# Kernel tuning notes

Hardware: AMD Instinct MI355X
Metric: run time of the kernel (lower is better)

Reference implementation:

```python
import jax, jax.numpy as jnp
import numpy as np

N_NODES = 100000
N_EDGES = 1600000
IN_FEAT = 64
OUT_FEAT = 64


def setup_inputs() -> dict:
    key = jax.random.key(0)
    k_h, k_src, k_dst, k_w, k_b = jax.random.split(key, 5)
    h = jax.random.normal(k_h, (N_NODES, IN_FEAT), dtype=jnp.float32)
    src = jax.random.randint(k_src, (N_EDGES,), 0, N_NODES, dtype=jnp.int64)
    dst = jax.random.randint(k_dst, (N_EDGES,), 0, N_NODES, dtype=jnp.int64)
    # nn.Linear(in_feat*2, out_feat): weight [out, 2*in], bias [out]
    W = jax.random.normal(k_w, (OUT_FEAT, 2 * IN_FEAT), dtype=jnp.float32) * 0.05
    b = jax.random.normal(k_b, (OUT_FEAT,), dtype=jnp.float32) * 0.05
    return {"h": h, "src": src, "dst": dst, "W": W, "b": b}


def reference(h, src, dst, W, b):
    # message = copy_u: gather source-node features along edges  [E, F]
    msgs = h[src]
    # mean reduce per destination node (DGL mean -> 0 for isolated nodes)
    summed = jax.ops.segment_sum(msgs, dst, num_segments=N_NODES)  # [N, F]
    deg = jax.ops.segment_sum(jnp.ones((src.shape[0],), dtype=h.dtype), dst,
                              num_segments=N_NODES)                # [N]
    h_N = summed / jnp.maximum(deg, 1.0)[:, None]
    h_total = jnp.concatenate([h, h_N], axis=1)                    # [N, 2F]
    return h_total @ W.T + b
```

## Files before the change

### kernel.cpp

```cpp
#include <hip/hip_runtime.h>

#define IN_FEAT 64
#define OUT_FEAT 64
#define CAP 48
#define NB 196
#define BUFCAP 64
#define QPAD 16
#define ROUTE_BLOCKS 256

typedef __attribute__((ext_vector_type(8))) _Float16 half8;
typedef __attribute__((ext_vector_type(4))) float floatx4;
typedef __attribute__((ext_vector_type(4))) int intx4;

__global__ __launch_bounds__(256) void conv_kernel(const float* __restrict__ h,
        _Float16* __restrict__ h16, int total8, int* __restrict__ qtail) {
    int t = blockIdx.x * 256 + threadIdx.x;
    if (t < (NB * QPAD) / 4) ((intx4*)qtail)[t] = (intx4){0, 0, 0, 0};
    if (t >= total8) return;
    const float4* p = (const float4*)(h + (long long)t * 8);
    float4 a = p[0], c = p[1];
    half8 v;
    v[0] = (_Float16)a.x; v[1] = (_Float16)a.y;
    v[2] = (_Float16)a.z; v[3] = (_Float16)a.w;
    v[4] = (_Float16)c.x; v[5] = (_Float16)c.y;
    v[6] = (_Float16)c.z; v[7] = (_Float16)c.w;
    *(half8*)(h16 + (long long)t * 8) = v;
}

__global__ __launch_bounds__(512) void route_kernel(const int* __restrict__ src,
        const int* __restrict__ dst, int* __restrict__ qtail,
        int* __restrict__ queue, int E, int qcap, int epb) {
    __shared__ int cnt[NB];
    __shared__ int sbase[NB];
    __shared__ __align__(16) int buf[NB * BUFCAP];
    int tid = threadIdx.x;
    int eb = blockIdx.x * epb;
    int ee = eb + epb; if (ee > E) ee = E;
    for (int r0 = eb; r0 < ee; r0 += 512 * 8) {
        for (int i = tid; i < NB; i += 512) cnt[i] = 0;
        __syncthreads();
#pragma unroll
        for (int k = 0; k < 8; ++k) {
            int e = r0 + k * 512 + tid;
            if (e < ee) {
                int d = dst[e];
                int s = src[e];
                int b = d >> 9;
                int entry = ((d & 511) << 17) | s;
                int pos = atomicAdd(&cnt[b], 1);
                if (pos < BUFCAP) buf[b * BUFCAP + pos] = entry;
                else {
                    int p2 = atomicAdd(&qtail[b * QPAD], 1);
                    if (p2 < qcap) queue[(long long)b * qcap + p2] = entry;
                }
            }
        }
        __syncthreads();
        if (tid < NB) {
            int n = cnt[tid]; if (n > BUFCAP) n = BUFCAP;
            sbase[tid] = (n > 0) ? atomicAdd(&qtail[tid * QPAD], n) : 0;
        }
        __syncthreads();
        int w = tid >> 6, lane = tid & 63;
        int b1 = w * 25 + 25; if (b1 > NB) b1 = NB;
        for (int b = w * 25; b < b1; ++b) {
            int n = cnt[b]; if (n > BUFCAP) n = BUFCAP;
            if (lane < n) {
                int p = sbase[b] + lane;
                if (p < qcap) queue[(long long)b * qcap + p] = buf[b * BUFCAP + lane];
            }
        }
        __syncthreads();
    }
}

__global__ __launch_bounds__(512, 1) void build_kernel(const int* __restrict__ qtail,
        const int* __restrict__ queue, int* __restrict__ deg,
        int* __restrict__ csr, int N, int qcap) {
    __shared__ __align__(16) int lcsr[512 * CAP];
    __shared__ int ldeg[512];
    int tid = threadIdx.x;
    int bid = blockIdx.x;
    if (tid < 512) ldeg[tid] = 0;
    __syncthreads();
    int qn = qtail[bid * QPAD]; if (qn > qcap) qn = qcap;
    long long qb = (long long)bid * qcap;
    for (int i = tid; i < qn; i += 512) {
        int e = queue[qb + i];
        int dl = e >> 17;
        int s = e & 0x1FFFF;
        int pos = atomicAdd(&ldeg[dl], 1);
        if (pos < CAP) lcsr[dl * CAP + pos] = s;
    }
    __syncthreads();
    int base_node = bid << 9;
    int nn = N - base_node; if (nn > 512) nn = 512;
    if (nn <= 0) return;
    for (int i4 = tid; i4 < nn * (CAP / 4); i4 += 512) {
        int r = i4 / (CAP / 4), c4 = i4 % (CAP / 4);
        intx4 v = *(intx4*)&lcsr[r * CAP + c4 * 4];
        *(intx4*)&csr[((long long)(base_node + r) << 6) + c4 * 4] = v;
    }
    for (int i = tid; i < nn; i += 512) deg[base_node + i] = ldeg[i];
}

__global__ __launch_bounds__(256) void gather_kernel(const _Float16* __restrict__ h16,
        const int* __restrict__ deg, int* csr_x, int N) {
    int wave = threadIdx.x >> 6;
    int lane = threadIdx.x & 63;
    int n0 = (blockIdx.x * 4 + wave) * 4;
    if (n0 >= N) return;
#pragma unroll
    for (int it = 0; it < 2; ++it) {
        int a = n0 + it * 2;
        if (a >= N) return;
        int bn = a + 1;
        bool hasB = bn < N;
        int cntA = deg[a];
        int cntB = hasB ? deg[bn] : 0;
        int rawA = csr_x[(a << 6) | lane];
        int rawB = hasB ? csr_x[(bn << 6) | lane] : 0;
        _Float16 selfA = h16[(long long)a * IN_FEAT + lane];
        _Float16 selfB = hasB ? h16[(long long)bn * IN_FEAT + lane] : (_Float16)0.0f;
        int mA = cntA < CAP ? cntA : CAP;
        int mB = cntB < CAP ? cntB : CAP;
        int sidA = (lane < mA) ? rawA : 0;
        int sidB = (lane < mB) ? rawB : 0;
        float accA0 = 0.f, accA1 = 0.f, accB0 = 0.f, accB1 = 0.f;
        int mmax = mA > mB ? mA : mB;
        for (int j = 0; j < mmax; j += 8) {
            float va[8], vb[8];
#pragma unroll
            for (int k = 0; k < 8; ++k) {
                int sA = __shfl(sidA, j + k);
                int sB = __shfl(sidB, j + k);
                va[k] = (float)h16[(long long)sA * IN_FEAT + lane];
                vb[k] = (float)h16[(long long)sB * IN_FEAT + lane];
            }
#pragma unroll
            for (int k = 0; k < 8; ++k) {
                float xa = (j + k < mA) ? va[k] : 0.0f;
                float xb = (j + k < mB) ? vb[k] : 0.0f;
                if (k & 1) { accA1 += xa; accB1 += xb; }
                else       { accA0 += xa; accB0 += xb; }
            }
        }
        float meanA = (accA0 + accA1) / fmaxf((float)cntA, 1.0f);
        _Float16* xrA = (_Float16*)(csr_x + ((long long)a << 6));
        xrA[lane] = selfA;
        xrA[IN_FEAT + lane] = (_Float16)meanA;
        if (hasB) {
            float meanB = (accB0 + accB1) / fmaxf((float)cntB, 1.0f);
            _Float16* xrB = (_Float16*)(csr_x + ((long long)bn << 6));
            xrB[lane] = selfB;
            xrB[IN_FEAT + lane] = (_Float16)meanB;
        }
    }
}

__global__ __launch_bounds__(256) void linear_kernel(const int* __restrict__ x_i,
        const float* __restrict__ W, const float* __restrict__ b,
        float* __restrict__ out, int N) {
    const _Float16* x = (const _Float16*)x_i;
    __shared__ _Float16 wlds[16 * 64 * 8];
    int wave = threadIdx.x >> 6;
    int lane = threadIdx.x & 63;
    int quad = lane >> 4;
    int l16  = lane & 15;

    for (int i = threadIdx.x; i < 64 * 2 * IN_FEAT; i += 256) {
        int row = i >> 7, col = i & 127;
        int t = row >> 4, lr = row & 15;
        int q = col >> 5, qd = (col & 31) >> 3, j = col & 7;
        wlds[(((t * 4 + q) * 64) + (qd * 16 + lr)) * 8 + j] = (_Float16)W[i];
    }
    __syncthreads();

    int node_base = (blockIdx.x * 4 + wave) * 16;
    if (node_base >= N) return;

    half8 bf[4][4];
#pragma unroll
    for (int t = 0; t < 4; ++t)
#pragma unroll
        for (int q = 0; q < 4; ++q)
            bf[t][q] = *(const half8*)&wlds[((t * 4 + q) * 64 + lane) * 8];
    float bias[4];
#pragma unroll
    for (int t = 0; t < 4; ++t) bias[t] = b[16 * t + l16];

    int mrow = node_base + l16;
    if (mrow >= N) mrow = N - 1;

    floatx4 z = {0.0f, 0.0f, 0.0f, 0.0f};
    floatx4 acc[4] = {z, z, z, z};
#pragma unroll
    for (int q = 0; q < 4; ++q) {
        half8 af = *(const half8*)&x[(long long)mrow * (2 * IN_FEAT) + 32 * q + 8 * quad];
#pragma unroll
        for (int t = 0; t < 4; ++t)
            acc[t] = __builtin_amdgcn_mfma_f32_16x16x32_f16(af, bf[t][q], acc[t], 0, 0, 0);
    }
#pragma unroll
    for (int t = 0; t < 4; ++t)
#pragma unroll
        for (int r = 0; r < 4; ++r) {
            int n = node_base + quad * 4 + r;
            if (n < N)
                out[(long long)n * OUT_FEAT + 16 * t + l16] = acc[t][r] + bias[t];
        }
}

extern "C" void kernel_launch(void* const* d_in, const int* in_sizes, int n_in,
                              void* d_out, int out_size, void* d_ws, size_t ws_size,
                              hipStream_t stream) {
    const float* h   = (const float*)d_in[0];
    const int*   src = (const int*)d_in[1];
    const int*   dst = (const int*)d_in[2];
    const float* W   = (const float*)d_in[3];
    const float* b   = (const float*)d_in[4];
    float* out = (float*)d_out;

    int N = in_sizes[0] / IN_FEAT;
    int E = in_sizes[1];

    int* deg   = (int*)d_ws;
    int* csr   = deg + N;
    int* qtail = csr + (size_t)N * 64;
    int* queue = qtail + NB * QPAD;
    _Float16* h16 = (_Float16*)out;

    int qcap = (int)((long long)E * 512 / N) + 1024;
    int epb  = (E + ROUTE_BLOCKS - 1) / ROUTE_BLOCKS;
    int nbr  = (N + 511) >> 9;

    int total8 = N * IN_FEAT / 8;
    conv_kernel<<<(total8 + 255) / 256, 256, 0, stream>>>(h, h16, total8, qtail);

    route_kernel<<<ROUTE_BLOCKS, 512, 0, stream>>>(src, dst, qtail, queue, E, qcap, epb);
    build_kernel<<<nbr, 512, 0, stream>>>(qtail, queue, deg, csr, N, qcap);

    int gather_blocks = (N + 15) / 16;
    gather_kernel<<<gather_blocks, 256, 0, stream>>>(h16, deg, csr, N);

    int tiles = (N + 15) / 16;
    linear_kernel<<<(tiles + 3) / 4, 256, 0, stream>>>(csr, W, b, out, N);
}
```

Measured before the change: 171.1 us.

## Halve destination bucket size and gather four nodes per wave concurrently

Destination buckets now cover 256 nodes instead of 512, giving 392 buckets. That doubles the number of route and build blocks and halves build_kernel's LDS footprint, so its launch bound is relaxed to allow more than one block per CU. The gather kernel now processes four nodes together in one interleaved neighbor loop, with per-node guards in place of the previous two sequential pairs. This is meant to expose more memory-level parallelism in the random h16 gathers and to improve occupancy of the CSR build. The trade-offs are more global atomic queue tails, smaller per-bucket LDS staging buffers that overflow to global atomics more often, and higher register pressure in gather.

```diff
diff --git a/kernel.cpp b/kernel.cpp
--- a/kernel.cpp
+++ b/kernel.cpp
@@ -3,10 +3,10 @@
 #define IN_FEAT 64
 #define OUT_FEAT 64
 #define CAP 48
-#define NB 196
-#define BUFCAP 64
+#define NB 392
+#define BUFCAP 32
 #define QPAD 16
-#define ROUTE_BLOCKS 256
+#define ROUTE_BLOCKS 512
 
 typedef __attribute__((ext_vector_type(8))) _Float16 half8;
 typedef __attribute__((ext_vector_type(4))) float floatx4;
@@ -45,8 +45,8 @@
             if (e < ee) {
                 int d = dst[e];
                 int s = src[e];
-                int b = d >> 9;
-                int entry = ((d & 511) << 17) | s;
+                int b = d >> 8;
+                int entry = ((d & 255) << 17) | s;
                 int pos = atomicAdd(&cnt[b], 1);
                 if (pos < BUFCAP) buf[b * BUFCAP + pos] = entry;
                 else {
@@ -62,8 +62,8 @@
         }
         __syncthreads();
         int w = tid >> 6, lane = tid & 63;
-        int b1 = w * 25 + 25; if (b1 > NB) b1 = NB;
-        for (int b = w * 25; b < b1; ++b) {
+        int b0 = w * 49, b1 = b0 + 49; if (b1 > NB) b1 = NB;
+        for (int b = b0; b < b1; ++b) {
             int n = cnt[b]; if (n > BUFCAP) n = BUFCAP;
             if (lane < n) {
                 int p = sbase[b] + lane;
@@ -74,14 +74,14 @@
     }
 }
 
-__global__ __launch_bounds__(512, 1) void build_kernel(const int* __restrict__ qtail,
+__global__ __launch_bounds__(512) void build_kernel(const int* __restrict__ qtail,
         const int* __restrict__ queue, int* __restrict__ deg,
         int* __restrict__ csr, int N, int qcap) {
-    __shared__ __align__(16) int lcsr[512 * CAP];
-    __shared__ int ldeg[512];
+    __shared__ __align__(16) int lcsr[256 * CAP];
+    __shared__ int ldeg[256];
     int tid = threadIdx.x;
     int bid = blockIdx.x;
-    if (tid < 512) ldeg[tid] = 0;
+    if (tid < 256) ldeg[tid] = 0;
     __syncthreads();
     int qn = qtail[bid * QPAD]; if (qn > qcap) qn = qcap;
     long long qb = (long long)bid * qcap;
@@ -93,8 +93,8 @@
         if (pos < CAP) lcsr[dl * CAP + pos] = s;
     }
     __syncthreads();
-    int base_node = bid << 9;
-    int nn = N - base_node; if (nn > 512) nn = 512;
+    int base_node = bid << 8;
+    int nn = N - base_node; if (nn > 256) nn = 256;
     if (nn <= 0) return;
     for (int i4 = tid; i4 < nn * (CAP / 4); i4 += 512) {
         int r = i4 / (CAP / 4), c4 = i4 % (CAP / 4);
@@ -110,50 +110,44 @@
     int lane = threadIdx.x & 63;
     int n0 = (blockIdx.x * 4 + wave) * 4;
     if (n0 >= N) return;
-#pragma unroll
-    for (int it = 0; it < 2; ++it) {
-        int a = n0 + it * 2;
-        if (a >= N) return;
-        int bn = a + 1;
-        bool hasB = bn < N;
-        int cntA = deg[a];
-        int cntB = hasB ? deg[bn] : 0;
-        int rawA = csr_x[(a << 6) | lane];
-        int rawB = hasB ? csr_x[(bn << 6) | lane] : 0;
-        _Float16 selfA = h16[(long long)a * IN_FEAT + lane];
-        _Float16 selfB = hasB ? h16[(long long)bn * IN_FEAT + lane] : (_Float16)0.0f;
-        int mA = cntA < CAP ? cntA : CAP;
-        int mB = cntB < CAP ? cntB : CAP;
-        int sidA = (lane < mA) ? rawA : 0;
-        int sidB = (lane < mB) ? rawB : 0;
-        float accA0 = 0.f, accA1 = 0.f, accB0 = 0.f, accB1 = 0.f;
-        int mmax = mA > mB ? mA : mB;
-        for (int j = 0; j < mmax; j += 8) {
-            float va[8], vb[8];
-#pragma unroll
-            for (int k = 0; k < 8; ++k) {
-                int sA = __shfl(sidA, j + k);
-                int sB = __shfl(sidB, j + k);
-                va[k] = (float)h16[(long long)sA * IN_FEAT + lane];
-                vb[k] = (float)h16[(long long)sB * IN_FEAT + lane];
+    int nc[4]; bool ok[4]; int cnt4[4], m4[4], sid4[4];
+    _Float16 self4[4];
+#pragma unroll
+    for (int c = 0; c < 4; ++c) {
+        int n = n0 + c;
+        ok[c] = n < N;
+        nc[c] = ok[c] ? n : N - 1;
+        cnt4[c] = deg[nc[c]];
+        int raw = csr_x[(nc[c] << 6) | lane];
+        self4[c] = h16[(long long)nc[c] * IN_FEAT + lane];
+        m4[c] = cnt4[c] < CAP ? cnt4[c] : CAP;
+        sid4[c] = (lane < m4[c]) ? raw : 0;
+    }
+    float acc[4][2];
+#pragma unroll
+    for (int c = 0; c < 4; ++c) { acc[c][0] = 0.f; acc[c][1] = 0.f; }
+    int mmax = 0;
+#pragma unroll
+    for (int c = 0; c < 4; ++c) if (ok[c] && m4[c] > mmax) mmax = m4[c];
+    for (int j = 0; j < mmax; j += 8) {
+#pragma unroll
+        for (int k = 0; k < 8; ++k) {
+#pragma unroll
+            for (int c = 0; c < 4; ++c) {
+                if (j + k < m4[c]) {
+                    int s = __shfl(sid4[c], j + k);
+                    acc[c][k & 1] += (float)h16[(long long)s * IN_FEAT + lane];
+                }
             }
-#pragma unroll
-            for (int k = 0; k < 8; ++k) {
-                float xa = (j + k < mA) ? va[k] : 0.0f;
-                float xb = (j + k < mB) ? vb[k] : 0.0f;
-                if (k & 1) { accA1 += xa; accB1 += xb; }
-                else       { accA0 += xa; accB0 += xb; }
-            }
-        }
-        float meanA = (accA0 + accA1) / fmaxf((float)cntA, 1.0f);
-        _Float16* xrA = (_Float16*)(csr_x + ((long long)a << 6));
-        xrA[lane] = selfA;
-        xrA[IN_FEAT + lane] = (_Float16)meanA;
-        if (hasB) {
-            float meanB = (accB0 + accB1) / fmaxf((float)cntB, 1.0f);
-            _Float16* xrB = (_Float16*)(csr_x + ((long long)bn << 6));
-            xrB[lane] = selfB;
-            xrB[IN_FEAT + lane] = (_Float16)meanB;
+        }
+    }
+#pragma unroll
+    for (int c = 0; c < 4; ++c) {
+        if (ok[c]) {
+            float mean = (acc[c][0] + acc[c][1]) / fmaxf((float)cnt4[c], 1.0f);
+            _Float16* xr = (_Float16*)(csr_x + ((long long)nc[c] << 6));
+            xr[lane] = self4[c];
+            xr[IN_FEAT + lane] = (_Float16)mean;
         }
     }
 }
@@ -230,9 +224,9 @@
     int* queue = qtail + NB * QPAD;
     _Float16* h16 = (_Float16*)out;
 
-    int qcap = (int)((long long)E * 512 / N) + 1024;
+    int qcap = (int)((long long)E * 256 / N) + 768;
     int epb  = (E + ROUTE_BLOCKS - 1) / ROUTE_BLOCKS;
-    int nbr  = (N + 511) >> 9;
+    int nbr  = (N + 255) >> 8;
 
     int total8 = N * IN_FEAT / 8;
     conv_kernel<<<(total8 + 255) / 256, 256, 0, stream>>>(h, h16, total8, qtail);
```

After: 236.1 us. +38.0%, slower.

## Fuse gather with linear layer and fold fp16 conversion into route kernel

Applied to the files above, without the earlier changes.

Merges the neighbor-mean gather and the MFMA linear layer into one kernel. Each wave builds 16 rows of the concatenated [self, mean] features in LDS and multiplies them directly, so the intermediate x rows are no longer written to and re-read from global memory. The fp16 conversion of h moves into the route kernel as a grid-stride prologue, and the queue-tail zeroing becomes a memset, which drops one launch. The fused path only runs when the workspace has room for a separate h16 buffer, otherwise it falls back to the old two-kernel path. The fused kernel also does more serial work per wave (16 nodes instead of 4) and uses more LDS.

```diff
diff --git a/kernel.cpp b/kernel.cpp
--- a/kernel.cpp
+++ b/kernel.cpp
@@ -7,29 +7,28 @@
 #define BUFCAP 64
 #define QPAD 16
 #define ROUTE_BLOCKS 256
+#define XSTR 136
 
 typedef __attribute__((ext_vector_type(8))) _Float16 half8;
 typedef __attribute__((ext_vector_type(4))) float floatx4;
 typedef __attribute__((ext_vector_type(4))) int intx4;
 
-__global__ __launch_bounds__(256) void conv_kernel(const float* __restrict__ h,
-        _Float16* __restrict__ h16, int total8, int* __restrict__ qtail) {
-    int t = blockIdx.x * 256 + threadIdx.x;
-    if (t < (NB * QPAD) / 4) ((intx4*)qtail)[t] = (intx4){0, 0, 0, 0};
-    if (t >= total8) return;
-    const float4* p = (const float4*)(h + (long long)t * 8);
-    float4 a = p[0], c = p[1];
-    half8 v;
-    v[0] = (_Float16)a.x; v[1] = (_Float16)a.y;
-    v[2] = (_Float16)a.z; v[3] = (_Float16)a.w;
-    v[4] = (_Float16)c.x; v[5] = (_Float16)c.y;
-    v[6] = (_Float16)c.z; v[7] = (_Float16)c.w;
-    *(half8*)(h16 + (long long)t * 8) = v;
-}
-
 __global__ __launch_bounds__(512) void route_kernel(const int* __restrict__ src,
         const int* __restrict__ dst, int* __restrict__ qtail,
-        int* __restrict__ queue, int E, int qcap, int epb) {
+        int* __restrict__ queue, int E, int qcap, int epb,
+        const float* __restrict__ h, _Float16* __restrict__ h16, int total8) {
+    for (int t = blockIdx.x * 512 + threadIdx.x; t < total8;
+         t += ROUTE_BLOCKS * 512) {
+        const float4* p = (const float4*)(h + (long long)t * 8);
+        float4 a = p[0], c = p[1];
+        half8 v;
+        v[0] = (_Float16)a.x; v[1] = (_Float16)a.y;
+        v[2] = (_Float16)a.z; v[3] = (_Float16)a.w;
+        v[4] = (_Float16)c.x; v[5] = (_Float16)c.y;
+        v[6] = (_Float16)c.z; v[7] = (_Float16)c.w;
+        *(half8*)(h16 + (long long)t * 8) = v;
+    }
+
     __shared__ int cnt[NB];
     __shared__ int sbase[NB];
     __shared__ __align__(16) int buf[NB * BUFCAP];
@@ -102,6 +101,100 @@
         *(intx4*)&csr[((long long)(base_node + r) << 6) + c4 * 4] = v;
     }
     for (int i = tid; i < nn; i += 512) deg[base_node + i] = ldeg[i];
+}
+
+__global__ __launch_bounds__(256) void gather_linear_kernel(
+        const _Float16* __restrict__ h16, const int* __restrict__ deg,
+        const int* __restrict__ csr, const float* __restrict__ W,
+        const float* __restrict__ b, float* __restrict__ out, int N) {
+    __shared__ _Float16 wlds[16 * 64 * 8];
+    __shared__ __align__(16) _Float16 xt[4][16 * XSTR];
+    int wave = threadIdx.x >> 6;
+    int lane = threadIdx.x & 63;
+    int quad = lane >> 4;
+    int l16  = lane & 15;
+
+    for (int i = threadIdx.x; i < 64 * 2 * IN_FEAT; i += 256) {
+        int row = i >> 7, col = i & 127;
+        int t = row >> 4, lr = row & 15;
+        int q = col >> 5, qd = (col & 31) >> 3, j = col & 7;
+        wlds[(((t * 4 + q) * 64) + (qd * 16 + lr)) * 8 + j] = (_Float16)W[i];
+    }
+
+    int nb = blockIdx.x * 64 + wave * 16;
+#pragma unroll
+    for (int it = 0; it < 8; ++it) {
+        int a = nb + it * 2;
+        int bn = a + 1;
+        bool okA = a < N, okB = bn < N;
+        int ca = okA ? a : 0, cb = okB ? bn : 0;
+        int cntA = okA ? deg[ca] : 0;
+        int cntB = okB ? deg[cb] : 0;
+        int rawA = okA ? csr[(ca << 6) | lane] : 0;
+        int rawB = okB ? csr[(cb << 6) | lane] : 0;
+        _Float16 selfA = okA ? h16[(long long)ca * IN_FEAT + lane] : (_Float16)0.0f;
+        _Float16 selfB = okB ? h16[(long long)cb * IN_FEAT + lane] : (_Float16)0.0f;
+        int mA = cntA < CAP ? cntA : CAP;
+        int mB = cntB < CAP ? cntB : CAP;
+        int sidA = (lane < mA) ? rawA : 0;
+        int sidB = (lane < mB) ? rawB : 0;
+        float accA0 = 0.f, accA1 = 0.f, accB0 = 0.f, accB1 = 0.f;
+        int mmax = mA > mB ? mA : mB;
+        for (int j = 0; j < mmax; j += 8) {
+            float va[8], vb[8];
+#pragma unroll
+            for (int k = 0; k < 8; ++k) {
+                int sA = __shfl(sidA, j + k);
+                int sB = __shfl(sidB, j + k);
+                va[k] = (float)h16[(long long)sA * IN_FEAT + lane];
+                vb[k] = (float)h16[(long long)sB * IN_FEAT + lane];
+            }
+#pragma unroll
+            for (int k = 0; k < 8; ++k) {
+                float xa = (j + k < mA) ? va[k] : 0.0f;
+                float xb = (j + k < mB) ? vb[k] : 0.0f;
+                if (k & 1) { accA1 += xa; accB1 += xb; }
+                else       { accA0 += xa; accB0 += xb; }
+            }
+        }
+        int rA = it * 2;
+        xt[wave][rA * XSTR + lane] = selfA;
+        xt[wave][rA * XSTR + IN_FEAT + lane] =
+            (_Float16)((accA0 + accA1) / fmaxf((float)cntA, 1.0f));
+        xt[wave][(rA + 1) * XSTR + lane] = selfB;
+        xt[wave][(rA + 1) * XSTR + IN_FEAT + lane] =
+            (_Float16)((accB0 + accB1) / fmaxf((float)cntB, 1.0f));
+    }
+    __syncthreads();
+
+    if (nb >= N) return;
+    half8 bf[4][4];
+#pragma unroll
+    for (int t = 0; t < 4; ++t)
+#pragma unroll
+        for (int q = 0; q < 4; ++q)
+            bf[t][q] = *(const half8*)&wlds[((t * 4 + q) * 64 + lane) * 8];
+    float bias[4];
+#pragma unroll
+    for (int t = 0; t < 4; ++t) bias[t] = b[16 * t + l16];
+
+    floatx4 z = {0.0f, 0.0f, 0.0f, 0.0f};
+    floatx4 acc[4] = {z, z, z, z};
+#pragma unroll
+    for (int q = 0; q < 4; ++q) {
+        half8 af = *(const half8*)&xt[wave][l16 * XSTR + 32 * q + 8 * quad];
+#pragma unroll
+        for (int t = 0; t < 4; ++t)
+            acc[t] = __builtin_amdgcn_mfma_f32_16x16x32_f16(af, bf[t][q], acc[t], 0, 0, 0);
+    }
+#pragma unroll
+    for (int t = 0; t < 4; ++t)
+#pragma unroll
+        for (int r = 0; r < 4; ++r) {
+            int n = nb + quad * 4 + r;
+            if (n < N)
+                out[(long long)n * OUT_FEAT + 16 * t + l16] = acc[t][r] + bias[t];
+        }
 }
 
 __global__ __launch_bounds__(256) void gather_kernel(const _Float16* __restrict__ h16,
@@ -167,7 +260,6 @@
     int lane = threadIdx.x & 63;
     int quad = lane >> 4;
     int l16  = lane & 15;
-
     for (int i = threadIdx.x; i < 64 * 2 * IN_FEAT; i += 256) {
         int row = i >> 7, col = i & 127;
         int t = row >> 4, lr = row & 15;
@@ -175,10 +267,8 @@
         wlds[(((t * 4 + q) * 64) + (qd * 16 + lr)) * 8 + j] = (_Float16)W[i];
     }
     __syncthreads();
-
     int node_base = (blockIdx.x * 4 + wave) * 16;
     if (node_base >= N) return;
-
     half8 bf[4][4];
 #pragma unroll
     for (int t = 0; t < 4; ++t)
@@ -188,10 +278,8 @@
     float bias[4];
 #pragma unroll
     for (int t = 0; t < 4; ++t) bias[t] = b[16 * t + l16];
-
     int mrow = node_base + l16;
     if (mrow >= N) mrow = N - 1;
-
     floatx4 z = {0.0f, 0.0f, 0.0f, 0.0f};
     floatx4 acc[4] = {z, z, z, z};
 #pragma unroll
@@ -224,25 +312,31 @@
     int N = in_sizes[0] / IN_FEAT;
     int E = in_sizes[1];
 
+    int qcap = (int)((long long)E * 512 / N) + 1024;
+    int epb  = (E + ROUTE_BLOCKS - 1) / ROUTE_BLOCKS;
+    int nbr  = (N + 511) >> 9;
+
     int* deg   = (int*)d_ws;
     int* csr   = deg + N;
     int* qtail = csr + (size_t)N * 64;
     int* queue = qtail + NB * QPAD;
-    _Float16* h16 = (_Float16*)out;
-
-    int qcap = (int)((long long)E * 512 / N) + 1024;
-    int epb  = (E + ROUTE_BLOCKS - 1) / ROUTE_BLOCKS;
-    int nbr  = (N + 511) >> 9;
+    size_t base_ints = (size_t)N * 65 + NB * QPAD + (size_t)NB * qcap;
+    bool fused = ws_size >= (base_ints + (size_t)N * 32) * sizeof(int);
+    _Float16* h16 = fused ? (_Float16*)(queue + (size_t)NB * qcap)
+                          : (_Float16*)out;
 
     int total8 = N * IN_FEAT / 8;
-    conv_kernel<<<(total8 + 255) / 256, 256, 0, stream>>>(h, h16, total8, qtail);
-
-    route_kernel<<<ROUTE_BLOCKS, 512, 0, stream>>>(src, dst, qtail, queue, E, qcap, epb);
+    (void)hipMemsetAsync(qtail, 0, (size_t)NB * QPAD * sizeof(int), stream);
+    route_kernel<<<ROUTE_BLOCKS, 512, 0, stream>>>(src, dst, qtail, queue,
+                                                   E, qcap, epb, h, h16, total8);
     build_kernel<<<nbr, 512, 0, stream>>>(qtail, queue, deg, csr, N, qcap);
 
-    int gather_blocks = (N + 15) / 16;
-    gather_kernel<<<gather_blocks, 256, 0, stream>>>(h16, deg, csr, N);
-
-    int tiles = (N + 15) / 16;
-    linear_kernel<<<(tiles + 3) / 4, 256, 0, stream>>>(csr, W, b, out, N);
-}
+    if (fused) {
+        gather_linear_kernel<<<(N + 63) / 64, 256, 0, stream>>>(
+            h16, deg, csr, W, b, out, N);
+    } else {
+        gather_kernel<<<(N + 15) / 16, 256, 0, stream>>>(h16, deg, csr, N);
+        int tiles = (N + 15) / 16;
+        linear_kernel<<<(tiles + 3) / 4, 256, 0, stream>>>(csr, W, b, out, N);
+    }
+}
```

New measurement: 174.1 us. Within noise of the previous version (+1.8%).
